# Kernel tuning notes

Measured on AMD Instinct MI355X. Metric: run time of the kernel, lower is better.

The kernel has to match this reference:

```python
import jax, jax.numpy as jnp
import numpy as np

B, T, C, H, W = 2, 8, 512, 32, 32
HEADS, HD = 8, 64          # head_dim = C // num_heads
GROUPS = 32                # GroupNorm_0 num_groups
EPS = 1e-6


def setup_inputs() -> dict:
    key = jax.random.key(0)
    k = jax.random.split(key, 5)
    return {
        "x": jax.random.normal(k[0], (B, T, C, H, W), jnp.float32),
        "gn_scale": jnp.ones((C,), jnp.float32),
        "gn_bias": jnp.zeros((C,), jnp.float32),
        "w_qkv": jax.random.normal(k[1], (C, 3 * C), jnp.float32) / float(np.sqrt(C)),
        "b_qkv": jnp.zeros((3 * C,), jnp.float32),
        "w_out": jax.random.normal(k[2], (C, C), jnp.float32) / float(np.sqrt(C)),
        "b_out": jnp.zeros((C,), jnp.float32),
    }


def reference(x, gn_scale, gn_bias, w_qkv, b_qkv, w_out, b_out):
    Bv, Tv, Cv, Hv, Wv = x.shape
    N = Bv * Tv
    xv = x.reshape(N, Cv, Hv, Wv)

    # GroupNorm(32 groups, eps=1e-6) with affine
    g = xv.reshape(N, GROUPS, Cv // GROUPS, Hv, Wv)
    mu = g.mean(axis=(2, 3, 4), keepdims=True)
    var = g.var(axis=(2, 3, 4), keepdims=True)
    hn = ((g - mu) * jax.lax.rsqrt(var + EPS)).reshape(N, Cv, Hv, Wv)
    hn = hn * gn_scale[None, :, None, None] + gn_bias[None, :, None, None]

    # NIN qkv projection (per-pixel 1x1): (N,C,H,W) x (C,3C) -> (N,3C,H,W)
    h = jnp.einsum('nchw,cd->ndhw', hn, w_qkv) + b_qkv[None, :, None, None]
    h = h.reshape(N, HEADS, 3 * HD, Hv * Wv).transpose(0, 1, 3, 2)  # (N,h,S,3d)
    q, k, v = jnp.split(h, 3, axis=-1)

    # naive scaled dot-product attention over S = H*W tokens
    logits = jnp.einsum('nhsd,nhtd->nhst', q, k) / float(np.sqrt(HD))
    attn = jax.nn.softmax(logits, axis=-1)
    vals = jnp.einsum('nhst,nhtd->nhsd', attn, v)

    h = vals.transpose(0, 1, 3, 2).reshape(N, Cv, Hv, Wv)
    # output NIN (init_scale=0 in torch; random params here) + residual
    h = jnp.einsum('nchw,cd->ndhw', h, w_out) + b_out[None, :, None, None]
    return x + h.reshape(Bv, Tv, Cv, Hv, Wv)
```

## Files before the change

### kernel.cpp

```cpp
#include <hip/hip_runtime.h>
#include <stdint.h>

typedef __bf16 bf16x8 __attribute__((ext_vector_type(8)));
typedef float f32x4v __attribute__((ext_vector_type(4)));
typedef float f32x16v __attribute__((ext_vector_type(16)));

__device__ __forceinline__ unsigned f2bf_rn(float f) {
    return (__float_as_uint(f) + 0x8000u) >> 16;
}
__device__ __forceinline__ unsigned pk2bf(float a, float b) {
    return __builtin_amdgcn_perm(__float_as_uint(b) + 0x8000u,
                                 __float_as_uint(a) + 0x8000u, 0x07060302u);
}

#define GLD_LDS16(gp, lp) __builtin_amdgcn_global_load_lds( \
    (const __attribute__((address_space(1))) unsigned int*)(gp), \
    (__attribute__((address_space(3))) unsigned int*)(lp), 16, 0, 0)

__global__ __launch_bounds__(256) void wt_kernel(const float* __restrict__ wqkv,
        const float* __restrict__ wout, unsigned short* __restrict__ WqT,
        unsigned short* __restrict__ WoT) {
    __shared__ float tile[32][33];
    int bx = blockIdx.x;
    const float* in; unsigned short* out; int Cc, c0;
    if (bx < 48) { in = wqkv; out = WqT; Cc = 1536; c0 = bx * 32; }
    else         { in = wout; out = WoT; Cc = 512;  c0 = (bx - 48) * 32; }
    int r0 = blockIdx.y * 32;
    int tx = threadIdx.x & 31, ty = threadIdx.x >> 5;
    #pragma unroll
    for (int i = 0; i < 4; i++) {
        int r = ty + i * 8;
        tile[r][tx] = in[(size_t)(r0 + r) * Cc + c0 + tx];
    }
    __syncthreads();
    #pragma unroll
    for (int i = 0; i < 4; i++) {
        int cr = ty + i * 8;
        out[(size_t)(c0 + cr) * 512 + r0 + tx] = (unsigned short)f2bf_rn(tile[tx][cr]);
    }
}

__global__ __launch_bounds__(256) void gn_kernel(const float* __restrict__ x,
        const float* __restrict__ scale, const float* __restrict__ bias,
        unsigned short* __restrict__ hnT) {
    int blk = blockIdx.x;
    int tid = threadIdx.x;
    int g = blk & 31, n = blk >> 5;
    const float4* src4 = (const float4*)(x + (size_t)blk * 16384);

    float s = 0.f, s2 = 0.f;
    for (int i = tid; i < 4096; i += 256) {
        float4 v = src4[i];
        s  += v.x + v.y + v.z + v.w;
        s2 += v.x*v.x + v.y*v.y + v.z*v.z + v.w*v.w;
    }
    __shared__ float red[256], red2[256];
    red[tid] = s; red2[tid] = s2;
    __syncthreads();
    for (int off = 128; off > 0; off >>= 1) {
        if (tid < off) { red[tid] += red[tid+off]; red2[tid] += red2[tid+off]; }
        __syncthreads();
    }
    __shared__ float sc_s[16], bi_s[16];
    if (tid < 16) {
        float mean = red[0] * (1.f/16384.f);
        float var  = red2[0] * (1.f/16384.f) - mean*mean;
        float rstd = rsqrtf(var + 1e-6f);
        int c = g*16 + tid;
        float sc = scale[c] * rstd;
        sc_s[tid] = sc;
        bi_s[tid] = bias[c] - mean * sc;
    }
    __shared__ float tile[16][260];
    for (int ch = 0; ch < 4; ch++) {
        __syncthreads();
        #pragma unroll
        for (int kk = 0; kk < 4; kk++) {
            int fi = tid + kk*256;
            int row = fi >> 6, col4 = fi & 63;
            float4 v = src4[row*256 + ch*64 + col4];
            *(float4*)&tile[row][col4*4] = v;
        }
        __syncthreads();
        int sQ = ch*256 + tid;
        unsigned int pk[8];
        #pragma unroll
        for (int c2 = 0; c2 < 8; c2++) {
            float a = tile[c2*2][tid]   * sc_s[c2*2]   + bi_s[c2*2];
            float b = tile[c2*2+1][tid] * sc_s[c2*2+1] + bi_s[c2*2+1];
            pk[c2] = pk2bf(a, b);
        }
        unsigned short* op = hnT + ((size_t)(n*1024 + sQ))*512 + g*16;
        *(uint4*)op       = make_uint4(pk[0], pk[1], pk[2], pk[3]);
        *((uint4*)op + 1) = make_uint4(pk[4], pk[5], pk[6], pk[7]);
    }
}

__global__ __launch_bounds__(256) void qkv_kernel(
        const unsigned short* __restrict__ WqT, const unsigned short* __restrict__ hnT,
        const float* __restrict__ bqkv,
        unsigned short* __restrict__ qb, unsigned short* __restrict__ kbuf,
        unsigned short* __restrict__ vb) {
    int s0 = blockIdx.x * 128, m0 = blockIdx.y * 128, n = blockIdx.z;
    __shared__ unsigned short At[4096];
    __shared__ unsigned short Bt[4096];
    int tid = threadIdx.x;
    int lane = tid & 63, w = tid >> 6;
    int quad = lane >> 4, tx = lane & 15;
    int moff = (w & 1) * 64, soff = (w >> 1) * 64;

    const unsigned short* Arow = WqT + (size_t)m0 * 512;
    const unsigned short* Brow = hnT + ((size_t)n * 1024 + s0) * 512;

    f32x4v acc[4][4];
    #pragma unroll
    for (int i = 0; i < 4; i++)
        #pragma unroll
        for (int j = 0; j < 4; j++)
            #pragma unroll
            for (int e = 0; e < 4; e++) acc[i][j][e] = 0.f;

    int f1 = tid, f2 = tid + 256;
    int m1 = f1 >> 2, kb1 = ((f1 & 3) - (f1 >> 3)) & 3;
    int m2 = f2 >> 2, kb2 = ((f2 & 3) - (f2 >> 3)) & 3;

    for (int k0 = 0; k0 < 512; k0 += 32) {
        __syncthreads();
        GLD_LDS16(Arow + (size_t)m1*512 + k0 + kb1*8, At + f1*8);
        GLD_LDS16(Arow + (size_t)m2*512 + k0 + kb2*8, At + f2*8);
        GLD_LDS16(Brow + (size_t)m1*512 + k0 + kb1*8, Bt + f1*8);
        GLD_LDS16(Brow + (size_t)m2*512 + k0 + kb2*8, Bt + f2*8);
        __syncthreads();
        bf16x8 af[4], bfr[4];
        #pragma unroll
        for (int mt = 0; mt < 4; mt++) {
            int m = moff + mt*16 + tx;
            int ch = m*4 + ((quad + (m >> 1)) & 3);
            af[mt] = *(const bf16x8*)(At + ch*8);
        }
        #pragma unroll
        for (int nt = 0; nt < 4; nt++) {
            int m = soff + nt*16 + tx;
            int ch = m*4 + ((quad + (m >> 1)) & 3);
            bfr[nt] = *(const bf16x8*)(Bt + ch*8);
        }
        #pragma unroll
        for (int mt = 0; mt < 4; mt++)
            #pragma unroll
            for (int nt = 0; nt < 4; nt++)
                acc[mt][nt] = __builtin_amdgcn_mfma_f32_16x16x32_bf16(
                    af[mt], bfr[nt], acc[mt][nt], 0, 0, 0);
    }

    const float QSCL = 0.18033688011112042f;
    #pragma unroll
    for (int mt = 0; mt < 4; mt++) {
        int m = m0 + moff + mt*16 + quad*4;
        int head = m / 192;
        int r = m - head*192;
        int which = r >> 6;
        int d0 = r & 63;
        float4 bia = *(const float4*)(bqkv + m);
        float scl = (which == 0) ? QSCL : 1.0f;
        #pragma unroll
        for (int nt = 0; nt < 4; nt++) {
            int sQ = s0 + soff + nt*16 + tx;
            f32x4v a = acc[mt][nt];
            float v0 = (a[0]+bia.x)*scl, v1 = (a[1]+bia.y)*scl;
            float v2 = (a[2]+bia.z)*scl, v3 = (a[3]+bia.w)*scl;
            if (which < 2) {
                unsigned short* base = (which == 0) ? qb : kbuf;
                unsigned lo = pk2bf(v0, v1), hi2 = pk2bf(v2, v3);
                *(uint2*)(base + (((size_t)(n*8 + head)*1024 + sQ) << 6) + d0) =
                    make_uint2(lo, hi2);
            } else {
                size_t vbase = ((size_t)(n*8 + head)*64 + d0)*1024 + sQ;
                vb[vbase]        = (unsigned short)f2bf_rn(v0);
                vb[vbase + 1024] = (unsigned short)f2bf_rn(v1);
                vb[vbase + 2048] = (unsigned short)f2bf_rn(v2);
                vb[vbase + 3072] = (unsigned short)f2bf_rn(v3);
            }
        }
    }
}

__global__ __launch_bounds__(256) void attn_kernel(
        const unsigned short* __restrict__ qg, const unsigned short* __restrict__ kg,
        const unsigned short* __restrict__ vg, unsigned short* __restrict__ ao) {
    int bid = blockIdx.x;
    int nh = bid & 127, qbk = bid >> 7;
    int tid = threadIdx.x, w = tid >> 6, lane = tid & 63;
    int lq = lane & 31, hi = lane >> 5;
    const unsigned short* Q = qg + (size_t)nh * 65536;
    const unsigned short* K = kg + (size_t)nh * 65536;
    const unsigned short* V = vg + (size_t)nh * 65536;

    __shared__ unsigned short Klds[64*72];
    __shared__ unsigned short Vlds[64*72];
    __shared__ unsigned short Plds[4][32*72];
    __shared__ float lsum_s[4][32];

    int q0 = qbk*128 + w*32;
    bf16x8 qf[4];
    #pragma unroll
    for (int ks = 0; ks < 4; ks++)
        qf[ks] = *(const bf16x8*)(Q + ((size_t)(q0 + lq))*64 + ks*16 + hi*8);

    f32x16v O0, O1;
    #pragma unroll
    for (int i = 0; i < 16; i++) { O0[i] = 0.f; O1[i] = 0.f; }
    float lsum = 0.f;

    for (int t0 = 0; t0 < 1024; t0 += 64) {
        __syncthreads();
        {
            int r = tid >> 2, part = (tid & 3) * 16;
            const uint4* kp = (const uint4*)(K + (size_t)(t0 + r)*64 + part);
            uint4 a = kp[0], b = kp[1];
            unsigned short* kd = Klds + r*72 + part;
            *(uint4*)kd = a; *(uint4*)(kd+8) = b;
            const uint4* vp = (const uint4*)(V + (size_t)r*1024 + t0 + part);
            uint4 c = vp[0], d = vp[1];
            unsigned short* vd = Vlds + r*72 + part;
            *(uint4*)vd = c; *(uint4*)(vd+8) = d;
        }
        __syncthreads();

        f32x16v S0, S1;
        #pragma unroll
        for (int i = 0; i < 16; i++) { S0[i] = 0.f; S1[i] = 0.f; }
        #pragma unroll
        for (int ks = 0; ks < 4; ks++) {
            bf16x8 a0 = *(const bf16x8*)(Klds + lq*72 + ks*16 + hi*8);
            bf16x8 a1 = *(const bf16x8*)(Klds + (32+lq)*72 + ks*16 + hi*8);
            S0 = __builtin_amdgcn_mfma_f32_32x32x16_bf16(a0, qf[ks], S0, 0, 0, 0);
            S1 = __builtin_amdgcn_mfma_f32_32x32x16_bf16(a1, qf[ks], S1, 0, 0, 0);
        }

        #pragma unroll
        for (int i = 0; i < 16; i++) {
            S0[i] = exp2f(S0[i]);
            S1[i] = exp2f(S1[i]);
            lsum += S0[i] + S1[i];
        }
        unsigned short* Pw = Plds[w];
        #pragma unroll
        for (int rq = 0; rq < 4; rq++) {
            unsigned a0 = pk2bf(S0[rq*4+0], S0[rq*4+1]);
            unsigned a1 = pk2bf(S0[rq*4+2], S0[rq*4+3]);
            unsigned b0 = pk2bf(S1[rq*4+0], S1[rq*4+1]);
            unsigned b1 = pk2bf(S1[rq*4+2], S1[rq*4+3]);
            *(uint2*)(Pw + lq*72 + rq*8 + hi*4)      = make_uint2(a0, a1);
            *(uint2*)(Pw + lq*72 + 32 + rq*8 + hi*4) = make_uint2(b0, b1);
        }

        #pragma unroll
        for (int ks = 0; ks < 4; ks++) {
            bf16x8 pa = *(const bf16x8*)(Pw + lq*72 + ks*16 + hi*8);
            bf16x8 v0 = *(const bf16x8*)(Vlds + lq*72 + ks*16 + hi*8);
            bf16x8 v1 = *(const bf16x8*)(Vlds + (32+lq)*72 + ks*16 + hi*8);
            O0 = __builtin_amdgcn_mfma_f32_32x32x16_bf16(pa, v0, O0, 0, 0, 0);
            O1 = __builtin_amdgcn_mfma_f32_32x32x16_bf16(pa, v1, O1, 0, 0, 0);
        }
    }

    lsum += __shfl_xor(lsum, 32);
    lsum_s[w][lq] = lsum;
    int n = nh >> 3, h = nh & 7;
    #pragma unroll
    for (int rq = 0; rq < 4; rq++) {
        float4 lv = *(const float4*)&lsum_s[w][rq*8 + hi*4];
        float invs[4] = {1.f/lv.x, 1.f/lv.y, 1.f/lv.z, 1.f/lv.w};
        #pragma unroll
        for (int i = 0; i < 4; i++) {
            int sQ = q0 + rq*8 + hi*4 + i;
            size_t rowb = ((size_t)(n*1024 + sQ))*512 + h*64;
            ao[rowb + lq]      = (unsigned short)f2bf_rn(O0[rq*4+i] * invs[i]);
            ao[rowb + 32 + lq] = (unsigned short)f2bf_rn(O1[rq*4+i] * invs[i]);
        }
    }
}

__global__ __launch_bounds__(256) void out_kernel(
        const unsigned short* __restrict__ aoT, const unsigned short* __restrict__ WoT,
        const float* __restrict__ bout, const float* __restrict__ x,
        float* __restrict__ out) {
    int s0 = blockIdx.x * 128, d0b = blockIdx.y * 128, n = blockIdx.z;
    __shared__ unsigned short At[4096];
    __shared__ unsigned short Bt[4096];
    int tid = threadIdx.x;
    int lane = tid & 63, w = tid >> 6;
    int quad = lane >> 4, tx = lane & 15;
    int moff = (w & 1) * 64, noff = (w >> 1) * 64;

    const unsigned short* Arow = aoT + ((size_t)n * 1024 + s0) * 512;
    const unsigned short* Brow = WoT + (size_t)d0b * 512;

    f32x4v acc[4][4];
    #pragma unroll
    for (int i = 0; i < 4; i++)
        #pragma unroll
        for (int j = 0; j < 4; j++)
            #pragma unroll
            for (int e = 0; e < 4; e++) acc[i][j][e] = 0.f;

    int f1 = tid, f2 = tid + 256;
    int m1 = f1 >> 2, kb1 = ((f1 & 3) - (f1 >> 3)) & 3;
    int m2 = f2 >> 2, kb2 = ((f2 & 3) - (f2 >> 3)) & 3;

    for (int k0 = 0; k0 < 512; k0 += 32) {
        __syncthreads();
        GLD_LDS16(Arow + (size_t)m1*512 + k0 + kb1*8, At + f1*8);
        GLD_LDS16(Arow + (size_t)m2*512 + k0 + kb2*8, At + f2*8);
        GLD_LDS16(Brow + (size_t)m1*512 + k0 + kb1*8, Bt + f1*8);
        GLD_LDS16(Brow + (size_t)m2*512 + k0 + kb2*8, Bt + f2*8);
        __syncthreads();
        bf16x8 af[4], bfr[4];
        #pragma unroll
        for (int mt = 0; mt < 4; mt++) {
            int m = moff + mt*16 + tx;
            int ch = m*4 + ((quad + (m >> 1)) & 3);
            af[mt] = *(const bf16x8*)(At + ch*8);
        }
        #pragma unroll
        for (int nt = 0; nt < 4; nt++) {
            int m = noff + nt*16 + tx;
            int ch = m*4 + ((quad + (m >> 1)) & 3);
            bfr[nt] = *(const bf16x8*)(Bt + ch*8);
        }
        #pragma unroll
        for (int mt = 0; mt < 4; mt++)
            #pragma unroll
            for (int nt = 0; nt < 4; nt++)
                acc[mt][nt] = __builtin_amdgcn_mfma_f32_16x16x32_bf16(
                    af[mt], bfr[nt], acc[mt][nt], 0, 0, 0);
    }

    #pragma unroll
    for (int mt = 0; mt < 4; mt++) {
        int sQ = s0 + moff + mt*16 + quad*4;
        #pragma unroll
        for (int nt = 0; nt < 4; nt++) {
            int d = d0b + noff + nt*16 + tx;
            float bo = bout[d];
            size_t base = ((size_t)n*512 + d)*1024 + sQ;
            float4 xv = *(const float4*)(x + base);
            f32x4v a = acc[mt][nt];
            float4 o = make_float4(a[0]+bo+xv.x, a[1]+bo+xv.y, a[2]+bo+xv.z, a[3]+bo+xv.w);
            *(float4*)(out + base) = o;
        }
    }
}

extern "C" void kernel_launch(void* const* d_in, const int* in_sizes, int n_in,
                              void* d_out, int out_size, void* d_ws, size_t ws_size,
                              hipStream_t stream) {
    const float* x    = (const float*)d_in[0];
    const float* gns  = (const float*)d_in[1];
    const float* gnb  = (const float*)d_in[2];
    const float* wqkv = (const float*)d_in[3];
    const float* bqkv = (const float*)d_in[4];
    const float* wout = (const float*)d_in[5];
    const float* bout = (const float*)d_in[6];
    float* out = (float*)d_out;

    char* p = (char*)d_ws;
    size_t off = 0;
    auto carve = [&](size_t bytes) {
        char* r = p + off;
        off = (off + bytes + 255) & ~(size_t)255;
        return r;
    };
    unsigned short* hnT = (unsigned short*)carve((size_t)16*1024*512*2);
    unsigned short* qb2 = (unsigned short*)carve((size_t)128*1024*64*2);
    unsigned short* kb2 = (unsigned short*)carve((size_t)128*1024*64*2);
    unsigned short* vb2 = (unsigned short*)carve((size_t)128*64*1024*2);
    unsigned short* aoT = (unsigned short*)carve((size_t)16*1024*512*2);
    unsigned short* WqT = (unsigned short*)carve((size_t)1536*512*2);
    unsigned short* WoT = (unsigned short*)carve((size_t)512*512*2);

    wt_kernel<<<dim3(64, 16), 256, 0, stream>>>(wqkv, wout, WqT, WoT);
    gn_kernel<<<dim3(512), 256, 0, stream>>>(x, gns, gnb, hnT);
    qkv_kernel<<<dim3(8, 12, 16), 256, 0, stream>>>(WqT, hnT, bqkv, qb2, kb2, vb2);
    attn_kernel<<<dim3(1024), 256, 0, stream>>>(qb2, kb2, vb2, aoT);
    out_kernel<<<dim3(8, 4, 16), 256, 0, stream>>>(aoT, WoT, bout, x, out);
}
```

Measured before the change: 246.1 us.

## Double-buffer K/V tiles with register prefetch and keep P in registers via permlane swap

K/V tiles are now double-buffered in LDS, with the next tile prefetched into registers while the current one is computed. This halves the barriers per iteration and hides global load latency. The softmax probability tile no longer goes through an LDS store and reload. It is repacked in registers with permlane32 swaps, falling back to shuffles, into the MFMA A-operand layout. The cost is higher register pressure and a dependence on the exact MFMA accumulator layout being correct.

```diff
diff --git a/kernel.cpp b/kernel.cpp
--- a/kernel.cpp
+++ b/kernel.cpp
@@ -4,6 +4,7 @@
 typedef __bf16 bf16x8 __attribute__((ext_vector_type(8)));
 typedef float f32x4v __attribute__((ext_vector_type(4)));
 typedef float f32x16v __attribute__((ext_vector_type(16)));
+typedef unsigned u32x2 __attribute__((ext_vector_type(2)));
 
 __device__ __forceinline__ unsigned f2bf_rn(float f) {
     return (__float_as_uint(f) + 0x8000u) >> 16;
@@ -11,6 +12,26 @@
 __device__ __forceinline__ unsigned pk2bf(float a, float b) {
     return __builtin_amdgcn_perm(__float_as_uint(b) + 0x8000u,
                                  __float_as_uint(a) + 0x8000u, 0x07060302u);
+}
+
+__device__ __forceinline__ void swap32(unsigned &a, unsigned &b) {
+#if __has_builtin(__builtin_amdgcn_permlane32_swap)
+    u32x2 r = __builtin_amdgcn_permlane32_swap(a, b, false, false);
+    a = r[0]; b = r[1];
+#else
+    unsigned pa = (unsigned)__shfl_xor((int)a, 32);
+    unsigned pb = (unsigned)__shfl_xor((int)b, 32);
+    bool hi = (threadIdx.x & 32) != 0;
+    unsigned na = hi ? pb : a;
+    unsigned nb = hi ? b : pa;
+    a = na; b = nb;
+#endif
+}
+
+__device__ __forceinline__ bf16x8 mk8(unsigned a, unsigned b, unsigned c, unsigned e) {
+    union { int4 i; bf16x8 v; } u;
+    u.i = make_int4((int)a, (int)b, (int)c, (int)e);
+    return u.v;
 }
 
 #define GLD_LDS16(gp, lp) __builtin_amdgcn_global_load_lds( \
@@ -195,9 +216,8 @@
     const unsigned short* K = kg + (size_t)nh * 65536;
     const unsigned short* V = vg + (size_t)nh * 65536;
 
-    __shared__ unsigned short Klds[64*72];
-    __shared__ unsigned short Vlds[64*72];
-    __shared__ unsigned short Plds[4][32*72];
+    __shared__ unsigned short Klds[2][64*72];
+    __shared__ unsigned short Vlds[2][64*72];
     __shared__ float lsum_s[4][32];
 
     int q0 = qbk*128 + w*32;
@@ -206,33 +226,44 @@
     for (int ks = 0; ks < 4; ks++)
         qf[ks] = *(const bf16x8*)(Q + ((size_t)(q0 + lq))*64 + ks*16 + hi*8);
 
+    int r = tid >> 2, part = (tid & 3) * 16;
+    uint4 ka, kb2, va, vb2;
+    ka  = *(const uint4*)(K + (size_t)r*64 + part);
+    kb2 = *(const uint4*)(K + (size_t)r*64 + part + 8);
+    va  = *(const uint4*)(V + (size_t)r*1024 + part);
+    vb2 = *(const uint4*)(V + (size_t)r*1024 + part + 8);
+
     f32x16v O0, O1;
     #pragma unroll
     for (int i = 0; i < 16; i++) { O0[i] = 0.f; O1[i] = 0.f; }
     float lsum = 0.f;
 
-    for (int t0 = 0; t0 < 1024; t0 += 64) {
-        __syncthreads();
+    for (int it = 0; it < 16; it++) {
+        int buf = it & 1;
         {
-            int r = tid >> 2, part = (tid & 3) * 16;
-            const uint4* kp = (const uint4*)(K + (size_t)(t0 + r)*64 + part);
-            uint4 a = kp[0], b = kp[1];
-            unsigned short* kd = Klds + r*72 + part;
-            *(uint4*)kd = a; *(uint4*)(kd+8) = b;
-            const uint4* vp = (const uint4*)(V + (size_t)r*1024 + t0 + part);
-            uint4 c = vp[0], d = vp[1];
-            unsigned short* vd = Vlds + r*72 + part;
-            *(uint4*)vd = c; *(uint4*)(vd+8) = d;
-        }
-        __syncthreads();
+            unsigned short* kd = Klds[buf] + r*72 + part;
+            *(uint4*)kd = ka; *(uint4*)(kd+8) = kb2;
+            unsigned short* vd = Vlds[buf] + r*72 + part;
+            *(uint4*)vd = va; *(uint4*)(vd+8) = vb2;
+        }
+        __syncthreads();
+        if (it < 15) {
+            int t0 = (it + 1) * 64;
+            ka  = *(const uint4*)(K + (size_t)(t0 + r)*64 + part);
+            kb2 = *(const uint4*)(K + (size_t)(t0 + r)*64 + part + 8);
+            va  = *(const uint4*)(V + (size_t)r*1024 + t0 + part);
+            vb2 = *(const uint4*)(V + (size_t)r*1024 + t0 + part + 8);
+        }
+        const unsigned short* Kb = Klds[buf];
+        const unsigned short* Vb = Vlds[buf];
 
         f32x16v S0, S1;
         #pragma unroll
         for (int i = 0; i < 16; i++) { S0[i] = 0.f; S1[i] = 0.f; }
         #pragma unroll
         for (int ks = 0; ks < 4; ks++) {
-            bf16x8 a0 = *(const bf16x8*)(Klds + lq*72 + ks*16 + hi*8);
-            bf16x8 a1 = *(const bf16x8*)(Klds + (32+lq)*72 + ks*16 + hi*8);
+            bf16x8 a0 = *(const bf16x8*)(Kb + lq*72 + ks*16 + hi*8);
+            bf16x8 a1 = *(const bf16x8*)(Kb + (32+lq)*72 + ks*16 + hi*8);
             S0 = __builtin_amdgcn_mfma_f32_32x32x16_bf16(a0, qf[ks], S0, 0, 0, 0);
             S1 = __builtin_amdgcn_mfma_f32_32x32x16_bf16(a1, qf[ks], S1, 0, 0, 0);
         }
@@ -243,22 +274,22 @@
             S1[i] = exp2f(S1[i]);
             lsum += S0[i] + S1[i];
         }
-        unsigned short* Pw = Plds[w];
-        #pragma unroll
-        for (int rq = 0; rq < 4; rq++) {
-            unsigned a0 = pk2bf(S0[rq*4+0], S0[rq*4+1]);
-            unsigned a1 = pk2bf(S0[rq*4+2], S0[rq*4+3]);
-            unsigned b0 = pk2bf(S1[rq*4+0], S1[rq*4+1]);
-            unsigned b1 = pk2bf(S1[rq*4+2], S1[rq*4+3]);
-            *(uint2*)(Pw + lq*72 + rq*8 + hi*4)      = make_uint2(a0, a1);
-            *(uint2*)(Pw + lq*72 + 32 + rq*8 + hi*4) = make_uint2(b0, b1);
-        }
-
-        #pragma unroll
-        for (int ks = 0; ks < 4; ks++) {
-            bf16x8 pa = *(const bf16x8*)(Pw + lq*72 + ks*16 + hi*8);
-            bf16x8 v0 = *(const bf16x8*)(Vlds + lq*72 + ks*16 + hi*8);
-            bf16x8 v1 = *(const bf16x8*)(Vlds + (32+lq)*72 + ks*16 + hi*8);
+        unsigned d[16];
+        #pragma unroll
+        for (int p2 = 0; p2 < 8; p2++) {
+            d[p2]     = pk2bf(S0[p2*2], S0[p2*2+1]);
+            d[8 + p2] = pk2bf(S1[p2*2], S1[p2*2+1]);
+        }
+        swap32(d[0],  d[2]);  swap32(d[1],  d[3]);
+        swap32(d[4],  d[6]);  swap32(d[5],  d[7]);
+        swap32(d[8],  d[10]); swap32(d[9],  d[11]);
+        swap32(d[12], d[14]); swap32(d[13], d[15]);
+
+        #pragma unroll
+        for (int kc = 0; kc < 4; kc++) {
+            bf16x8 pa = mk8(d[kc*4+0], d[kc*4+1], d[kc*4+2], d[kc*4+3]);
+            bf16x8 v0 = *(const bf16x8*)(Vb + lq*72 + kc*16 + hi*8);
+            bf16x8 v1 = *(const bf16x8*)(Vb + (32+lq)*72 + kc*16 + hi*8);
             O0 = __builtin_amdgcn_mfma_f32_32x32x16_bf16(pa, v0, O0, 0, 0, 0);
             O1 = __builtin_amdgcn_mfma_f32_32x32x16_bf16(pa, v1, O1, 0, 0, 0);
         }
```

Result: faster. 238.8 us (-3.0%).
